# Kernel optimization log

Measured on AMD Instinct MI355X. Metric: run time of the kernel, lower is better.

## Reference

```python
import jax, jax.numpy as jnp
import numpy as np

H, W, SCALE = 480, 640, 8  # full-res grid and coarse downsample factor (hw0_i/hw0_c)


def _struct_feats(pts, anchor_ids):
    """pts: [N, H*W, 3]; anchor_ids: [N, A] int -> [N, L, 4*A] with L=(H//SCALE)*(W//SCALE)."""
    N = pts.shape[0]
    coarse = pts.reshape(N, H, W, 3)[:, ::SCALE, ::SCALE, :].reshape(N, -1, 3)  # [N, L, 3]
    anchors = jnp.take_along_axis(pts, anchor_ids[:, :, None], axis=1)          # [N, A, 3]
    diff = coarse[:, :, None, :] - anchors[:, None, :, :]                        # [N, L, A, 3]
    dist = jnp.sum(diff * diff, axis=-1, keepdims=True)                          # [N, L, A, 1]
    s = jnp.concatenate([diff, dist], axis=-1)                                   # [N, L, A, 4]
    s = s / jnp.sum(jnp.abs(s), axis=-2, keepdims=True)                          # L1 norm over anchor axis
    s = jnp.swapaxes(s, -1, -2).reshape(N, coarse.shape[1], -1)                  # [N, L, 4A]
    return s


def _mlp(x, W1, b1, W2, b2):
    return jax.nn.relu(x @ W1 + b1) @ W2 + b2


def setup_inputs() -> dict:
    key = jax.random.key(0)
    ks = jax.random.split(key, 10)
    N, L, C, A, P = 4, 4800, 256, 128, H * W
    D = C + 4 * A  # 768
    return {
        "feat0": jax.random.normal(ks[0], (N, L, C), jnp.float32),
        "feat1": jax.random.normal(ks[1], (N, L, C), jnp.float32),
        "pts_3d0": jax.random.normal(ks[2], (N, P, 3), jnp.float32),
        "pts_3d1": jax.random.normal(ks[3], (N, P, 3), jnp.float32),
        "anchor_i_ids": jax.random.randint(ks[4], (N, A), 0, P),
        "anchor_j_ids": jax.random.randint(ks[5], (N, A), 0, P),
        "W1": jax.random.normal(ks[6], (D, D), jnp.float32) * (1.0 / np.sqrt(D)),
        "b1": jnp.zeros((D,), jnp.float32),
        "W2": jax.random.normal(ks[7], (D, C), jnp.float32) * (1.0 / np.sqrt(D)),
        "b2": jnp.zeros((C,), jnp.float32),
    }


def reference(feat0, feat1, pts_3d0, pts_3d1, anchor_i_ids, anchor_j_ids, W1, b1, W2, b2):
    s0 = _struct_feats(pts_3d0, anchor_i_ids)  # [N, L, 4A]
    s1 = _struct_feats(pts_3d1, anchor_j_ids)
    aug0 = _mlp(jnp.concatenate([feat0, s0], axis=-1), W1, b1, W2, b2)  # [N, L, C]
    aug1 = _mlp(jnp.concatenate([feat1, s1], axis=-1), W1, b1, W2, b2)
    return (aug0, aug1)
```

## Files before the change

kernel.cpp:

```cpp
#include <hip/hip_runtime.h>
#include <stdint.h>
#include <stddef.h>

typedef __attribute__((ext_vector_type(8))) short short8;
typedef __attribute__((ext_vector_type(4))) short short4v;
typedef __attribute__((ext_vector_type(4))) float f32x4;

typedef const __attribute__((address_space(3))) char* lds_cp;

#define GLDS16(gp, lp)                                                        \
    __builtin_amdgcn_global_load_lds(                                         \
        (const __attribute__((address_space(1))) void*)(gp),                  \
        (__attribute__((address_space(3))) void*)(lp), 16, 0, 0)

__device__ __forceinline__ short8 ldsr16(lds_cp p) {
    short8 v;
    asm volatile("ds_read_b128 %0, %1" : "=v"(v) : "v"(p));
    return v;
}

template <int N>
__device__ __forceinline__ void wait_lgkm() {
    static_assert(N == 0 || N == 2 || N == 4 || N == 8, "unsupported count");
    if constexpr (N == 0) asm volatile("s_waitcnt lgkmcnt(0)" ::: "memory");
    else if constexpr (N == 2) asm volatile("s_waitcnt lgkmcnt(2)" ::: "memory");
    else if constexpr (N == 4) asm volatile("s_waitcnt lgkmcnt(4)" ::: "memory");
    else if constexpr (N == 8) asm volatile("s_waitcnt lgkmcnt(8)" ::: "memory");
    __builtin_amdgcn_sched_barrier(0);
}

__device__ __forceinline__ unsigned short f2bf(float f) {
    union { float f; uint32_t u; } v;
    v.f = f;
    uint32_t u = v.u;
    u += 0x7FFFu + ((u >> 16) & 1u);
    return (unsigned short)(u >> 16);
}

__global__ __launch_bounds__(1024) void transpose_to_bf16(
    const float* __restrict__ src, unsigned short* __restrict__ dst, int R, int C)
{
    __shared__ float tile[32][33];
    const int c0 = blockIdx.x * 32, r0 = blockIdx.y * 32;
    const int tx = threadIdx.x, ty = threadIdx.y;
    tile[ty][tx] = src[(size_t)(r0 + ty) * C + (c0 + tx)];
    __syncthreads();
    dst[(size_t)(c0 + ty) * R + (r0 + tx)] = f2bf(tile[tx][ty]);
}

__global__ __launch_bounds__(64) void struct_pack(
    const float* __restrict__ feat0, const float* __restrict__ feat1,
    const float* __restrict__ pts0,  const float* __restrict__ pts1,
    const int* __restrict__ ids0,    const int* __restrict__ ids1,
    unsigned short* __restrict__ xw)
{
    const int m = blockIdx.x;
    const int t = m / 19200;
    const int r = m % 19200;
    const int n = r / 4800;
    const int l = r % 4800;
    const float* feat = t ? feat1 : feat0;
    const float* pts  = (t ? pts1 : pts0) + (size_t)n * (307200 * 3);
    const int*   ids  = (t ? ids1 : ids0) + n * 128;
    const int a = threadIdx.x;

    const int lr = l / 80, lc = l % 80;
    const int p  = (lr * 8) * 640 + lc * 8;
    const float cx = pts[p * 3 + 0], cy = pts[p * 3 + 1], cz = pts[p * 3 + 2];

    const int id0 = ids[a], id1 = ids[a + 64];
    const float d0x = cx - pts[id0 * 3 + 0];
    const float d0y = cy - pts[id0 * 3 + 1];
    const float d0z = cz - pts[id0 * 3 + 2];
    const float d0d = d0x * d0x + d0y * d0y + d0z * d0z;
    const float d1x = cx - pts[id1 * 3 + 0];
    const float d1y = cy - pts[id1 * 3 + 1];
    const float d1z = cz - pts[id1 * 3 + 2];
    const float d1d = d1x * d1x + d1y * d1y + d1z * d1z;

    float p0 = fabsf(d0x) + fabsf(d1x);
    float p1 = fabsf(d0y) + fabsf(d1y);
    float p2 = fabsf(d0z) + fabsf(d1z);
    float p3 = d0d + d1d;
#pragma unroll
    for (int off = 32; off; off >>= 1) {
        p0 += __shfl_xor(p0, off);
        p1 += __shfl_xor(p1, off);
        p2 += __shfl_xor(p2, off);
        p3 += __shfl_xor(p3, off);
    }
    const float i0 = 1.0f / p0, i1 = 1.0f / p1, i2 = 1.0f / p2, i3 = 1.0f / p3;

    unsigned short* xrow = xw + (size_t)m * 768;
    const float* frow = feat + (size_t)(n * 4800 + l) * 256;
    const float4 fv = ((const float4*)frow)[a];
    short4v s4;
    s4.x = (short)f2bf(fv.x); s4.y = (short)f2bf(fv.y);
    s4.z = (short)f2bf(fv.z); s4.w = (short)f2bf(fv.w);
    *(short4v*)(xrow + a * 4) = s4;

    xrow[256 + 0 * 128 + a]      = f2bf(d0x * i0);
    xrow[256 + 0 * 128 + a + 64] = f2bf(d1x * i0);
    xrow[256 + 1 * 128 + a]      = f2bf(d0y * i1);
    xrow[256 + 1 * 128 + a + 64] = f2bf(d1y * i1);
    xrow[256 + 2 * 128 + a]      = f2bf(d0z * i2);
    xrow[256 + 2 * 128 + a + 64] = f2bf(d1z * i2);
    xrow[256 + 3 * 128 + a]      = f2bf(d0d * i3);
    xrow[256 + 3 * 128 + a + 64] = f2bf(d1d * i3);
}

template <int MI, int NJ, int WRN_LOG, bool RELU, bool OUT_BF16>
__global__ __launch_bounds__(512, 2) void gemm_t(
    const unsigned short* __restrict__ A,
    const unsigned short* __restrict__ Bt,
    const float* __restrict__ bias,
    void* __restrict__ Cout,
    int K, int N, int ntx, int q8, int r8)
{
    constexpr int WRN = 1 << WRN_LOG;
    constexpr int WRM = 8 / WRN;
    constexpr int BM = WRM * MI * 16;
    constexpr int BN = WRN * NJ * 16;
    constexpr int ASLOT = BM * 128;
    constexpr int BSLOT = BN * 128;
    constexpr int ALD = BM / 64;
    constexpr int BLD = BN / 64;
    static_assert(ALD == 4, "vmcnt immediates assume 4 A-loads/wave/tile");
    static_assert(MI + NJ <= 13, "lgkm in-flight cap");

    extern __shared__ char lds[];
    const int nt = K >> 6;

    const int bid = blockIdx.x;
    const int xcd = bid & 7, idx = bid >> 3;
    const int w = (xcd < r8 ? xcd * (q8 + 1) : r8 * (q8 + 1) + (xcd - r8) * q8) + idx;
    const int n0 = (w % ntx) * BN;
    const int m0 = (w / ntx) * BM;

    const int tid = threadIdx.x;
    const int lane = tid & 63;
    const int wv = tid >> 6;
    const int wr = wv >> WRN_LOG;
    const int wc = wv & (WRN - 1);

    const int slr = lane >> 3;
    const int kc  = (lane & 7) ^ slr;
    const unsigned short* gA = A  + (size_t)(m0 + wv * 8 + slr) * K + kc * 8;
    const unsigned short* gB = Bt + (size_t)(n0 + wv * 8 + slr) * K + kc * 8;

    auto stA = [&](int slot, int i, int kt) {
        GLDS16(gA + (size_t)i * 64 * K + kt, lds + slot * ASLOT + (i * 64 + wv * 8) * 128);
    };
    auto stB = [&](int slot, int j, int kt) {
        GLDS16(gB + (size_t)j * 64 * K + kt, lds + 3 * ASLOT + slot * BSLOT + (j * 64 + wv * 8) * 128);
    };

    const int rsel = lane & 15;
    const int kbh  = lane >> 4;
    const int ck0 = ((kbh) ^ (rsel & 7)) * 16;
    const int ck1 = ((4 + kbh) ^ (rsel & 7)) * 16;
    const int aRowB = (wr * (MI * 16) + rsel) * 128;
    const int bRowB = (wc * (NJ * 16) + rsel) * 128;

    auto LDA = [&](int slot, int mi, int ks) -> short8 {
        return ldsr16((lds_cp)(lds + slot * ASLOT + aRowB + mi * 2048 + (ks ? ck1 : ck0)));
    };
    auto LDB = [&](int slot, int nj, int ks) -> short8 {
        return ldsr16((lds_cp)(lds + 3 * ASLOT + slot * BSLOT + bRowB + nj * 2048 + (ks ? ck1 : ck0)));
    };

    f32x4 acc[MI][NJ] = {};
    short8 aL[MI / 2], aH[MI / 2], aL1[MI / 2], aH1[MI / 2], bF0[NJ], bF1[NJ];

    {
#pragma unroll
        for (int i = 0; i < ALD; ++i) stA(0, i, 0);
#pragma unroll
        for (int j = 0; j < BLD; ++j) stB(0, j, 0);
        if (nt > 1) {
#pragma unroll
            for (int i = 0; i < ALD; ++i) stA(1, i, 64);
            asm volatile("s_waitcnt vmcnt(4)" ::: "memory");
        } else {
            asm volatile("s_waitcnt vmcnt(0)" ::: "memory");
        }
        __builtin_amdgcn_s_barrier();
    }

    int cb3 = 0;
    for (int t = 0; t < nt; ++t) {
        const int cb2 = t & 1;
        const int sb2 = cb2 ^ 1;
        int sa3 = cb3 + 2; if (sa3 >= 3) sa3 -= 3;
        const int kt1 = (t + 1) << 6;
        const int kt2 = (t + 2) << 6;
        const bool stb = (t + 1) < nt;
        const bool sta = (t + 2) < nt;

#pragma unroll
        for (int nj = 0; nj < NJ; ++nj) bF0[nj] = LDB(cb2, nj, 0);
#pragma unroll
        for (int mi = 0; mi < MI / 2; ++mi) aL[mi] = LDA(cb3, mi, 0);
#pragma unroll
        for (int mi = 0; mi < MI / 2; ++mi) aH[mi] = LDA(cb3, MI / 2 + mi, 0);

        wait_lgkm<MI / 2>();
        __builtin_amdgcn_s_setprio(1);
#pragma unroll
        for (int mi = 0; mi < MI / 2; ++mi)
#pragma unroll
            for (int nj = 0; nj < NJ; ++nj)
                acc[mi][nj] = __builtin_amdgcn_mfma_f32_16x16x32_bf16(aL[mi], bF0[nj], acc[mi][nj], 0, 0, 0);
        __builtin_amdgcn_s_setprio(0);

#pragma unroll
        for (int nj = 0; nj < NJ; ++nj) bF1[nj] = LDB(cb2, nj, 1);
        if (stb) {
#pragma unroll
            for (int j = 0; j < BLD; ++j) stB(sb2, j, kt1);
        }

        wait_lgkm<NJ>();
        __builtin_amdgcn_s_setprio(1);
#pragma unroll
        for (int mi = 0; mi < MI / 2; ++mi)
#pragma unroll
            for (int nj = 0; nj < NJ; ++nj)
                acc[MI / 2 + mi][nj] = __builtin_amdgcn_mfma_f32_16x16x32_bf16(aH[mi], bF0[nj], acc[MI / 2 + mi][nj], 0, 0, 0);
        __builtin_amdgcn_s_setprio(0);

#pragma unroll
        for (int mi = 0; mi < MI / 2; ++mi) aL1[mi] = LDA(cb3, mi, 1);
#pragma unroll
        for (int mi = 0; mi < MI / 2; ++mi) aH1[mi] = LDA(cb3, MI / 2 + mi, 1);
        if (sta) {
            stA(sa3, 0, kt2); stA(sa3, 1, kt2); stA(sa3, 2, kt2); stA(sa3, 3, kt2);
        }

        wait_lgkm<MI / 2>();
        __builtin_amdgcn_s_setprio(1);
#pragma unroll
        for (int mi = 0; mi < MI / 2; ++mi)
#pragma unroll
            for (int nj = 0; nj < NJ; ++nj)
                acc[mi][nj] = __builtin_amdgcn_mfma_f32_16x16x32_bf16(aL1[mi], bF1[nj], acc[mi][nj], 0, 0, 0);
        __builtin_amdgcn_s_setprio(0);

        wait_lgkm<0>();
        __builtin_amdgcn_s_setprio(1);
#pragma unroll
        for (int mi = 0; mi < MI / 2; ++mi)
#pragma unroll
            for (int nj = 0; nj < NJ; ++nj)
                acc[MI / 2 + mi][nj] = __builtin_amdgcn_mfma_f32_16x16x32_bf16(aH1[mi], bF1[nj], acc[MI / 2 + mi][nj], 0, 0, 0);
        __builtin_amdgcn_s_setprio(0);

        if (t + 1 < nt) {
            if (sta) asm volatile("s_waitcnt vmcnt(4)" ::: "memory");
            else     asm volatile("s_waitcnt vmcnt(0)" ::: "memory");
            __builtin_amdgcn_s_barrier();
        }
        cb3 = (cb3 + 1 == 3) ? 0 : cb3 + 1;
    }

    const int crow = (lane >> 4) * 4;
    const int ccol = lane & 15;
#pragma unroll
    for (int nj = 0; nj < NJ; ++nj) {
        const int col = n0 + wc * (NJ * 16) + nj * 16 + ccol;
        const float bv = bias[col];
#pragma unroll
        for (int mi = 0; mi < MI; ++mi) {
#pragma unroll
            for (int rg = 0; rg < 4; ++rg) {
                const int row = m0 + wr * (MI * 16) + mi * 16 + crow + rg;
                float v = acc[mi][nj][rg] + bv;
                if (RELU) v = fmaxf(v, 0.0f);
                if (OUT_BF16) {
                    ((unsigned short*)Cout)[(size_t)row * N + col] = f2bf(v);
                } else {
                    ((float*)Cout)[(size_t)row * N + col] = v;
                }
            }
        }
    }
}

extern "C" void kernel_launch(void* const* d_in, const int* in_sizes, int n_in,
                              void* d_out, int out_size, void* d_ws, size_t ws_size,
                              hipStream_t stream) {
    const float* feat0 = (const float*)d_in[0];
    const float* feat1 = (const float*)d_in[1];
    const float* pts0  = (const float*)d_in[2];
    const float* pts1  = (const float*)d_in[3];
    const int*   ids0  = (const int*)d_in[4];
    const int*   ids1  = (const int*)d_in[5];
    const float* W1    = (const float*)d_in[6];
    const float* b1    = (const float*)d_in[7];
    const float* W2    = (const float*)d_in[8];
    const float* b2    = (const float*)d_in[9];
    float* out = (float*)d_out;

    char* ws = (char*)d_ws;
    unsigned short* xw  = (unsigned short*)(ws);
    unsigned short* h   = (unsigned short*)(ws + 58982400);
    unsigned short* w1t = (unsigned short*)(ws + 117964800);
    unsigned short* w2t = (unsigned short*)(ws + 119144448);

    const int LDS1 = 3 * 32768 + 2 * 32768;
    const int LDS2 = 3 * 32768 + 2 * 16384;
    (void)hipFuncSetAttribute((const void*)&gemm_t<8, 4, 2, true, true>,
                              hipFuncAttributeMaxDynamicSharedMemorySize, LDS1);
    (void)hipFuncSetAttribute((const void*)&gemm_t<4, 4, 1, false, false>,
                              hipFuncAttributeMaxDynamicSharedMemorySize, LDS2);

    dim3 tb(32, 32);
    transpose_to_bf16<<<dim3(768 / 32, 768 / 32), tb, 0, stream>>>(W1, w1t, 768, 768);
    transpose_to_bf16<<<dim3(256 / 32, 768 / 32), tb, 0, stream>>>(W2, w2t, 768, 256);

    struct_pack<<<38400, 64, 0, stream>>>(feat0, feat1, pts0, pts1, ids0, ids1, xw);

    gemm_t<8, 4, 2, true, true><<<450, 512, LDS1, stream>>>(xw, w1t, b1, (void*)h, 768, 768, 3, 56, 2);
    gemm_t<4, 4, 1, false, false><<<300, 512, LDS2, stream>>>(h, w2t, b2, (void*)out, 768, 256, 2, 37, 4);
}
```

Measured before the change: 116.9 us.

## Unify GEMMs on a 256x128 tile with 4 waves and K-step of 32

Both MLP GEMMs now use a single 256x128 block tile run by 4 waves (each wave computes 128x64), with the K step halved from 64 to 32. The LDS layout and swizzle are rebuilt for 64-byte rows, and the per-iteration schedule is simplified to one batch of fragment loads followed by two MFMA phases. The first GEMM goes from 450 large blocks to 900 smaller ones, and the LDS footprint shrinks, which should allow more resident blocks. In exchange each block does more barriers per unit of work and has less data reuse per wave than the larger 8-wave tile.

```diff
diff --git a/kernel.cpp b/kernel.cpp
--- a/kernel.cpp
+++ b/kernel.cpp
@@ -21,11 +21,9 @@
 
 template <int N>
 __device__ __forceinline__ void wait_lgkm() {
-    static_assert(N == 0 || N == 2 || N == 4 || N == 8, "unsupported count");
+    static_assert(N == 0 || N == 4, "unsupported count");
     if constexpr (N == 0) asm volatile("s_waitcnt lgkmcnt(0)" ::: "memory");
-    else if constexpr (N == 2) asm volatile("s_waitcnt lgkmcnt(2)" ::: "memory");
-    else if constexpr (N == 4) asm volatile("s_waitcnt lgkmcnt(4)" ::: "memory");
-    else if constexpr (N == 8) asm volatile("s_waitcnt lgkmcnt(8)" ::: "memory");
+    else asm volatile("s_waitcnt lgkmcnt(4)" ::: "memory");
     __builtin_amdgcn_sched_barrier(0);
 }
 
@@ -109,77 +107,65 @@
     xrow[256 + 3 * 128 + a + 64] = f2bf(d1d * i3);
 }
 
-template <int MI, int NJ, int WRN_LOG, bool RELU, bool OUT_BF16>
-__global__ __launch_bounds__(512, 2) void gemm_t(
+template <bool RELU, bool OUT_BF16>
+__global__ __launch_bounds__(256, 2) void gemm_t(
     const unsigned short* __restrict__ A,
     const unsigned short* __restrict__ Bt,
     const float* __restrict__ bias,
     void* __restrict__ Cout,
     int K, int N, int ntx, int q8, int r8)
 {
-    constexpr int WRN = 1 << WRN_LOG;
-    constexpr int WRM = 8 / WRN;
-    constexpr int BM = WRM * MI * 16;
-    constexpr int BN = WRN * NJ * 16;
-    constexpr int ASLOT = BM * 128;
-    constexpr int BSLOT = BN * 128;
-    constexpr int ALD = BM / 64;
-    constexpr int BLD = BN / 64;
-    static_assert(ALD == 4, "vmcnt immediates assume 4 A-loads/wave/tile");
-    static_assert(MI + NJ <= 13, "lgkm in-flight cap");
-
+    constexpr int ASLOT = 256 * 64;
+    constexpr int BSLOT = 128 * 64;
     extern __shared__ char lds[];
-    const int nt = K >> 6;
+    char* ldsB = lds + 3 * ASLOT;
+    const int nt = K >> 5;
 
     const int bid = blockIdx.x;
     const int xcd = bid & 7, idx = bid >> 3;
     const int w = (xcd < r8 ? xcd * (q8 + 1) : r8 * (q8 + 1) + (xcd - r8) * q8) + idx;
-    const int n0 = (w % ntx) * BN;
-    const int m0 = (w / ntx) * BM;
+    const int n0 = (w % ntx) * 128;
+    const int m0 = (w / ntx) * 256;
 
     const int tid = threadIdx.x;
     const int lane = tid & 63;
     const int wv = tid >> 6;
-    const int wr = wv >> WRN_LOG;
-    const int wc = wv & (WRN - 1);
-
-    const int slr = lane >> 3;
-    const int kc  = (lane & 7) ^ slr;
-    const unsigned short* gA = A  + (size_t)(m0 + wv * 8 + slr) * K + kc * 8;
-    const unsigned short* gB = Bt + (size_t)(n0 + wv * 8 + slr) * K + kc * 8;
+    const int wr = wv >> 1;
+    const int wc = wv & 1;
+
+    const int lrow = lane >> 2;
+    const int lchk = (lane & 3) ^ ((lane >> 3) & 3);
+    const unsigned short* gA = A  + (size_t)(m0 + wv * 64 + lrow) * K + lchk * 8;
+    const unsigned short* gB = Bt + (size_t)(n0 + wv * 32 + lrow) * K + lchk * 8;
 
     auto stA = [&](int slot, int i, int kt) {
-        GLDS16(gA + (size_t)i * 64 * K + kt, lds + slot * ASLOT + (i * 64 + wv * 8) * 128);
+        GLDS16(gA + (size_t)i * 16 * K + kt, lds + slot * ASLOT + (wv * 4 + i) * 1024);
     };
     auto stB = [&](int slot, int j, int kt) {
-        GLDS16(gB + (size_t)j * 64 * K + kt, lds + 3 * ASLOT + slot * BSLOT + (j * 64 + wv * 8) * 128);
-    };
-
-    const int rsel = lane & 15;
-    const int kbh  = lane >> 4;
-    const int ck0 = ((kbh) ^ (rsel & 7)) * 16;
-    const int ck1 = ((4 + kbh) ^ (rsel & 7)) * 16;
-    const int aRowB = (wr * (MI * 16) + rsel) * 128;
-    const int bRowB = (wc * (NJ * 16) + rsel) * 128;
-
-    auto LDA = [&](int slot, int mi, int ks) -> short8 {
-        return ldsr16((lds_cp)(lds + slot * ASLOT + aRowB + mi * 2048 + (ks ? ck1 : ck0)));
-    };
-    auto LDB = [&](int slot, int nj, int ks) -> short8 {
-        return ldsr16((lds_cp)(lds + 3 * ASLOT + slot * BSLOT + bRowB + nj * 2048 + (ks ? ck1 : ck0)));
-    };
-
-    f32x4 acc[MI][NJ] = {};
-    short8 aL[MI / 2], aH[MI / 2], aL1[MI / 2], aH1[MI / 2], bF0[NJ], bF1[NJ];
+        GLDS16(gB + (size_t)j * 16 * K + kt, ldsB + slot * BSLOT + (wv * 2 + j) * 1024);
+    };
+
+    const int R = lane & 15;
+    const int q = lane >> 4;
+    const int ck = (q ^ ((R >> 1) & 3)) * 16;
+    const int aOff = (wr * 128 + R) * 64 + ck;
+    const int bOff = (wc * 64 + R) * 64 + ck;
+
+    auto LDA = [&](int slot, int mi) -> short8 {
+        return ldsr16((lds_cp)(lds + slot * ASLOT + aOff + mi * 1024));
+    };
+    auto LDB = [&](int slot, int nj) -> short8 {
+        return ldsr16((lds_cp)(ldsB + slot * BSLOT + bOff + nj * 1024));
+    };
+
+    f32x4 acc[8][4] = {};
+    short8 aF[8], bF[4];
 
     {
-#pragma unroll
-        for (int i = 0; i < ALD; ++i) stA(0, i, 0);
-#pragma unroll
-        for (int j = 0; j < BLD; ++j) stB(0, j, 0);
+        stA(0, 0, 0); stA(0, 1, 0); stA(0, 2, 0); stA(0, 3, 0);
+        stB(0, 0, 0); stB(0, 1, 0);
         if (nt > 1) {
-#pragma unroll
-            for (int i = 0; i < ALD; ++i) stA(1, i, 64);
+            stA(1, 0, 32); stA(1, 1, 32); stA(1, 2, 32); stA(1, 3, 32);
             asm volatile("s_waitcnt vmcnt(4)" ::: "memory");
         } else {
             asm volatile("s_waitcnt vmcnt(0)" ::: "memory");
@@ -192,67 +178,34 @@
         const int cb2 = t & 1;
         const int sb2 = cb2 ^ 1;
         int sa3 = cb3 + 2; if (sa3 >= 3) sa3 -= 3;
-        const int kt1 = (t + 1) << 6;
-        const int kt2 = (t + 2) << 6;
+        const int kt1 = (t + 1) << 5;
+        const int kt2 = (t + 2) << 5;
         const bool stb = (t + 1) < nt;
         const bool sta = (t + 2) < nt;
 
-#pragma unroll
-        for (int nj = 0; nj < NJ; ++nj) bF0[nj] = LDB(cb2, nj, 0);
-#pragma unroll
-        for (int mi = 0; mi < MI / 2; ++mi) aL[mi] = LDA(cb3, mi, 0);
-#pragma unroll
-        for (int mi = 0; mi < MI / 2; ++mi) aH[mi] = LDA(cb3, MI / 2 + mi, 0);
-
-        wait_lgkm<MI / 2>();
+        bF[0] = LDB(cb2, 0); bF[1] = LDB(cb2, 1); bF[2] = LDB(cb2, 2); bF[3] = LDB(cb2, 3);
+        aF[0] = LDA(cb3, 0); aF[1] = LDA(cb3, 1); aF[2] = LDA(cb3, 2); aF[3] = LDA(cb3, 3);
+        if (stb) { stB(sb2, 0, kt1); stB(sb2, 1, kt1); }
+
+        aF[4] = LDA(cb3, 4); aF[5] = LDA(cb3, 5); aF[6] = LDA(cb3, 6); aF[7] = LDA(cb3, 7);
+        if (sta) { stA(sa3, 0, kt2); stA(sa3, 1, kt2); stA(sa3, 2, kt2); stA(sa3, 3, kt2); }
+
+        wait_lgkm<4>();
         __builtin_amdgcn_s_setprio(1);
 #pragma unroll
-        for (int mi = 0; mi < MI / 2; ++mi)
-#pragma unroll
-            for (int nj = 0; nj < NJ; ++nj)
-                acc[mi][nj] = __builtin_amdgcn_mfma_f32_16x16x32_bf16(aL[mi], bF0[nj], acc[mi][nj], 0, 0, 0);
-        __builtin_amdgcn_s_setprio(0);
-
-#pragma unroll
-        for (int nj = 0; nj < NJ; ++nj) bF1[nj] = LDB(cb2, nj, 1);
-        if (stb) {
-#pragma unroll
-            for (int j = 0; j < BLD; ++j) stB(sb2, j, kt1);
-        }
-
-        wait_lgkm<NJ>();
-        __builtin_amdgcn_s_setprio(1);
-#pragma unroll
-        for (int mi = 0; mi < MI / 2; ++mi)
-#pragma unroll
-            for (int nj = 0; nj < NJ; ++nj)
-                acc[MI / 2 + mi][nj] = __builtin_amdgcn_mfma_f32_16x16x32_bf16(aH[mi], bF0[nj], acc[MI / 2 + mi][nj], 0, 0, 0);
-        __builtin_amdgcn_s_setprio(0);
-
-#pragma unroll
-        for (int mi = 0; mi < MI / 2; ++mi) aL1[mi] = LDA(cb3, mi, 1);
-#pragma unroll
-        for (int mi = 0; mi < MI / 2; ++mi) aH1[mi] = LDA(cb3, MI / 2 + mi, 1);
-        if (sta) {
-            stA(sa3, 0, kt2); stA(sa3, 1, kt2); stA(sa3, 2, kt2); stA(sa3, 3, kt2);
-        }
-
-        wait_lgkm<MI / 2>();
-        __builtin_amdgcn_s_setprio(1);
-#pragma unroll
-        for (int mi = 0; mi < MI / 2; ++mi)
-#pragma unroll
-            for (int nj = 0; nj < NJ; ++nj)
-                acc[mi][nj] = __builtin_amdgcn_mfma_f32_16x16x32_bf16(aL1[mi], bF1[nj], acc[mi][nj], 0, 0, 0);
+        for (int mi = 0; mi < 4; ++mi)
+#pragma unroll
+            for (int nj = 0; nj < 4; ++nj)
+                acc[mi][nj] = __builtin_amdgcn_mfma_f32_16x16x32_bf16(aF[mi], bF[nj], acc[mi][nj], 0, 0, 0);
         __builtin_amdgcn_s_setprio(0);
 
         wait_lgkm<0>();
         __builtin_amdgcn_s_setprio(1);
 #pragma unroll
-        for (int mi = 0; mi < MI / 2; ++mi)
-#pragma unroll
-            for (int nj = 0; nj < NJ; ++nj)
-                acc[MI / 2 + mi][nj] = __builtin_amdgcn_mfma_f32_16x16x32_bf16(aH1[mi], bF1[nj], acc[MI / 2 + mi][nj], 0, 0, 0);
+        for (int mi = 4; mi < 8; ++mi)
+#pragma unroll
+            for (int nj = 0; nj < 4; ++nj)
+                acc[mi][nj] = __builtin_amdgcn_mfma_f32_16x16x32_bf16(aF[mi], bF[nj], acc[mi][nj], 0, 0, 0);
         __builtin_amdgcn_s_setprio(0);
 
         if (t + 1 < nt) {
@@ -266,14 +219,14 @@
     const int crow = (lane >> 4) * 4;
     const int ccol = lane & 15;
 #pragma unroll
-    for (int nj = 0; nj < NJ; ++nj) {
-        const int col = n0 + wc * (NJ * 16) + nj * 16 + ccol;
+    for (int nj = 0; nj < 4; ++nj) {
+        const int col = n0 + wc * 64 + nj * 16 + ccol;
         const float bv = bias[col];
 #pragma unroll
-        for (int mi = 0; mi < MI; ++mi) {
+        for (int mi = 0; mi < 8; ++mi) {
 #pragma unroll
             for (int rg = 0; rg < 4; ++rg) {
-                const int row = m0 + wr * (MI * 16) + mi * 16 + crow + rg;
+                const int row = m0 + wr * 128 + mi * 16 + crow + rg;
                 float v = acc[mi][nj][rg] + bv;
                 if (RELU) v = fmaxf(v, 0.0f);
                 if (OUT_BF16) {
@@ -307,12 +260,11 @@
     unsigned short* w1t = (unsigned short*)(ws + 117964800);
     unsigned short* w2t = (unsigned short*)(ws + 119144448);
 
-    const int LDS1 = 3 * 32768 + 2 * 32768;
-    const int LDS2 = 3 * 32768 + 2 * 16384;
-    (void)hipFuncSetAttribute((const void*)&gemm_t<8, 4, 2, true, true>,
-                              hipFuncAttributeMaxDynamicSharedMemorySize, LDS1);
-    (void)hipFuncSetAttribute((const void*)&gemm_t<4, 4, 1, false, false>,
-                              hipFuncAttributeMaxDynamicSharedMemorySize, LDS2);
+    const int LDS = 3 * 16384 + 2 * 8192;
+    (void)hipFuncSetAttribute((const void*)&gemm_t<true, true>,
+                              hipFuncAttributeMaxDynamicSharedMemorySize, LDS);
+    (void)hipFuncSetAttribute((const void*)&gemm_t<false, false>,
+                              hipFuncAttributeMaxDynamicSharedMemorySize, LDS);
 
     dim3 tb(32, 32);
     transpose_to_bf16<<<dim3(768 / 32, 768 / 32), tb, 0, stream>>>(W1, w1t, 768, 768);
@@ -320,6 +272,6 @@
 
     struct_pack<<<38400, 64, 0, stream>>>(feat0, feat1, pts0, pts1, ids0, ids1, xw);
 
-    gemm_t<8, 4, 2, true, true><<<450, 512, LDS1, stream>>>(xw, w1t, b1, (void*)h, 768, 768, 3, 56, 2);
-    gemm_t<4, 4, 1, false, false><<<300, 512, LDS2, stream>>>(h, w2t, b2, (void*)out, 768, 256, 2, 37, 4);
-}
+    gemm_t<true, true><<<900, 256, LDS, stream>>>(xw, w1t, b1, (void*)h, 768, 768, 6, 112, 4);
+    gemm_t<false, false><<<300, 256, LDS, stream>>>(h, w2t, b2, (void*)out, 768, 256, 2, 37, 4);
+}
```

Result: no change. 116.0 us (-0.8%).

## Switch GEMM inner loop to 32x32x16 bf16 MFMA with 2x4 wave grid

Applied to the files above, without the earlier changes.

Replaces the 16x16x32 MFMA tiles with 32x32x16 MFMA tiles and a fixed 2x4 wave layout (each wave covers 128 rows by BFR*32 columns). The K-step of 64 is now split into four 16-wide substeps with double-buffered fragment registers and adjusted LDS swizzle offsets and wait counts. The aim is fewer LDS fragment reads per FLOP and higher MFMA throughput per instruction. The cost is larger accumulator register footprint and a different epilogue row mapping.

```diff
diff --git a/kernel.cpp b/kernel.cpp
--- a/kernel.cpp
+++ b/kernel.cpp
@@ -4,7 +4,7 @@
 
 typedef __attribute__((ext_vector_type(8))) short short8;
 typedef __attribute__((ext_vector_type(4))) short short4v;
-typedef __attribute__((ext_vector_type(4))) float f32x4;
+typedef __attribute__((ext_vector_type(16))) float f32x16;
 
 typedef const __attribute__((address_space(3))) char* lds_cp;
 
@@ -21,11 +21,10 @@
 
 template <int N>
 __device__ __forceinline__ void wait_lgkm() {
-    static_assert(N == 0 || N == 2 || N == 4 || N == 8, "unsupported count");
+    static_assert(N == 0 || N == 5 || N == 6, "unsupported count");
     if constexpr (N == 0) asm volatile("s_waitcnt lgkmcnt(0)" ::: "memory");
-    else if constexpr (N == 2) asm volatile("s_waitcnt lgkmcnt(2)" ::: "memory");
-    else if constexpr (N == 4) asm volatile("s_waitcnt lgkmcnt(4)" ::: "memory");
-    else if constexpr (N == 8) asm volatile("s_waitcnt lgkmcnt(8)" ::: "memory");
+    else if constexpr (N == 5) asm volatile("s_waitcnt lgkmcnt(5)" ::: "memory");
+    else if constexpr (N == 6) asm volatile("s_waitcnt lgkmcnt(6)" ::: "memory");
     __builtin_amdgcn_sched_barrier(0);
 }
 
@@ -109,7 +108,7 @@
     xrow[256 + 3 * 128 + a + 64] = f2bf(d1d * i3);
 }
 
-template <int MI, int NJ, int WRN_LOG, bool RELU, bool OUT_BF16>
+template <int AFR, int BFR, bool RELU, bool OUT_BF16>
 __global__ __launch_bounds__(512, 2) void gemm_t(
     const unsigned short* __restrict__ A,
     const unsigned short* __restrict__ Bt,
@@ -117,18 +116,17 @@
     void* __restrict__ Cout,
     int K, int N, int ntx, int q8, int r8)
 {
-    constexpr int WRN = 1 << WRN_LOG;
-    constexpr int WRM = 8 / WRN;
-    constexpr int BM = WRM * MI * 16;
-    constexpr int BN = WRN * NJ * 16;
+    constexpr int BM = 2 * AFR * 32;
+    constexpr int BN = 4 * BFR * 32;
     constexpr int ASLOT = BM * 128;
     constexpr int BSLOT = BN * 128;
     constexpr int ALD = BM / 64;
     constexpr int BLD = BN / 64;
+    constexpr int PERKS = AFR + BFR;
     static_assert(ALD == 4, "vmcnt immediates assume 4 A-loads/wave/tile");
-    static_assert(MI + NJ <= 13, "lgkm in-flight cap");
 
     extern __shared__ char lds[];
+    char* ldsB = lds + 3 * ASLOT;
     const int nt = K >> 6;
 
     const int bid = blockIdx.x;
@@ -140,8 +138,8 @@
     const int tid = threadIdx.x;
     const int lane = tid & 63;
     const int wv = tid >> 6;
-    const int wr = wv >> WRN_LOG;
-    const int wc = wv & (WRN - 1);
+    const int wr = wv >> 2;
+    const int wc = wv & 3;
 
     const int slr = lane >> 3;
     const int kc  = (lane & 7) ^ slr;
@@ -152,25 +150,26 @@
         GLDS16(gA + (size_t)i * 64 * K + kt, lds + slot * ASLOT + (i * 64 + wv * 8) * 128);
     };
     auto stB = [&](int slot, int j, int kt) {
-        GLDS16(gB + (size_t)j * 64 * K + kt, lds + 3 * ASLOT + slot * BSLOT + (j * 64 + wv * 8) * 128);
+        GLDS16(gB + (size_t)j * 64 * K + kt, ldsB + slot * BSLOT + (j * 64 + wv * 8) * 128);
     };
 
-    const int rsel = lane & 15;
-    const int kbh  = lane >> 4;
-    const int ck0 = ((kbh) ^ (rsel & 7)) * 16;
-    const int ck1 = ((4 + kbh) ^ (rsel & 7)) * 16;
-    const int aRowB = (wr * (MI * 16) + rsel) * 128;
-    const int bRowB = (wc * (NJ * 16) + rsel) * 128;
+    const int R32 = lane & 31;
+    const int hi  = lane >> 5;
+    int ck[4];
+#pragma unroll
+    for (int ks = 0; ks < 4; ++ks) ck[ks] = (((ks * 2 + hi) ^ (R32 & 7)) * 16);
+    const int aBase = (wr * 128 + R32) * 128;
+    const int bBase = (wc * (BFR * 32) + R32) * 128;
 
     auto LDA = [&](int slot, int mi, int ks) -> short8 {
-        return ldsr16((lds_cp)(lds + slot * ASLOT + aRowB + mi * 2048 + (ks ? ck1 : ck0)));
+        return ldsr16((lds_cp)(lds + slot * ASLOT + aBase + mi * 4096 + ck[ks]));
     };
     auto LDB = [&](int slot, int nj, int ks) -> short8 {
-        return ldsr16((lds_cp)(lds + 3 * ASLOT + slot * BSLOT + bRowB + nj * 2048 + (ks ? ck1 : ck0)));
+        return ldsr16((lds_cp)(ldsB + slot * BSLOT + bBase + nj * 4096 + ck[ks]));
     };
 
-    f32x4 acc[MI][NJ] = {};
-    short8 aL[MI / 2], aH[MI / 2], aL1[MI / 2], aH1[MI / 2], bF0[NJ], bF1[NJ];
+    f32x16 acc[AFR][BFR] = {};
+    short8 aF[2][AFR], bF[2][BFR];
 
     {
 #pragma unroll
@@ -198,61 +197,63 @@
         const bool sta = (t + 2) < nt;
 
 #pragma unroll
-        for (int nj = 0; nj < NJ; ++nj) bF0[nj] = LDB(cb2, nj, 0);
-#pragma unroll
-        for (int mi = 0; mi < MI / 2; ++mi) aL[mi] = LDA(cb3, mi, 0);
-#pragma unroll
-        for (int mi = 0; mi < MI / 2; ++mi) aH[mi] = LDA(cb3, MI / 2 + mi, 0);
-
-        wait_lgkm<MI / 2>();
-        __builtin_amdgcn_s_setprio(1);
-#pragma unroll
-        for (int mi = 0; mi < MI / 2; ++mi)
-#pragma unroll
-            for (int nj = 0; nj < NJ; ++nj)
-                acc[mi][nj] = __builtin_amdgcn_mfma_f32_16x16x32_bf16(aL[mi], bF0[nj], acc[mi][nj], 0, 0, 0);
-        __builtin_amdgcn_s_setprio(0);
-
-#pragma unroll
-        for (int nj = 0; nj < NJ; ++nj) bF1[nj] = LDB(cb2, nj, 1);
+        for (int mi = 0; mi < AFR; ++mi) aF[0][mi] = LDA(cb3, mi, 0);
+#pragma unroll
+        for (int nj = 0; nj < BFR; ++nj) bF[0][nj] = LDB(cb2, nj, 0);
+#pragma unroll
+        for (int mi = 0; mi < AFR; ++mi) aF[1][mi] = LDA(cb3, mi, 1);
+#pragma unroll
+        for (int nj = 0; nj < BFR; ++nj) bF[1][nj] = LDB(cb2, nj, 1);
         if (stb) {
 #pragma unroll
             for (int j = 0; j < BLD; ++j) stB(sb2, j, kt1);
         }
 
-        wait_lgkm<NJ>();
+        wait_lgkm<PERKS>();
         __builtin_amdgcn_s_setprio(1);
 #pragma unroll
-        for (int mi = 0; mi < MI / 2; ++mi)
-#pragma unroll
-            for (int nj = 0; nj < NJ; ++nj)
-                acc[MI / 2 + mi][nj] = __builtin_amdgcn_mfma_f32_16x16x32_bf16(aH[mi], bF0[nj], acc[MI / 2 + mi][nj], 0, 0, 0);
+        for (int mi = 0; mi < AFR; ++mi)
+#pragma unroll
+            for (int nj = 0; nj < BFR; ++nj)
+                acc[mi][nj] = __builtin_amdgcn_mfma_f32_32x32x16_bf16(aF[0][mi], bF[0][nj], acc[mi][nj], 0, 0, 0);
         __builtin_amdgcn_s_setprio(0);
 
 #pragma unroll
-        for (int mi = 0; mi < MI / 2; ++mi) aL1[mi] = LDA(cb3, mi, 1);
-#pragma unroll
-        for (int mi = 0; mi < MI / 2; ++mi) aH1[mi] = LDA(cb3, MI / 2 + mi, 1);
-        if (sta) {
-            stA(sa3, 0, kt2); stA(sa3, 1, kt2); stA(sa3, 2, kt2); stA(sa3, 3, kt2);
-        }
-
-        wait_lgkm<MI / 2>();
+        for (int mi = 0; mi < AFR; ++mi) aF[0][mi] = LDA(cb3, mi, 2);
+#pragma unroll
+        for (int nj = 0; nj < BFR; ++nj) bF[0][nj] = LDB(cb2, nj, 2);
+        if (sta) { stA(sa3, 0, kt2); stA(sa3, 1, kt2); stA(sa3, 2, kt2); stA(sa3, 3, kt2); }
+
+        wait_lgkm<PERKS>();
         __builtin_amdgcn_s_setprio(1);
 #pragma unroll
-        for (int mi = 0; mi < MI / 2; ++mi)
-#pragma unroll
-            for (int nj = 0; nj < NJ; ++nj)
-                acc[mi][nj] = __builtin_amdgcn_mfma_f32_16x16x32_bf16(aL1[mi], bF1[nj], acc[mi][nj], 0, 0, 0);
+        for (int mi = 0; mi < AFR; ++mi)
+#pragma unroll
+            for (int nj = 0; nj < BFR; ++nj)
+                acc[mi][nj] = __builtin_amdgcn_mfma_f32_32x32x16_bf16(aF[1][mi], bF[1][nj], acc[mi][nj], 0, 0, 0);
+        __builtin_amdgcn_s_setprio(0);
+
+#pragma unroll
+        for (int mi = 0; mi < AFR; ++mi) aF[1][mi] = LDA(cb3, mi, 3);
+#pragma unroll
+        for (int nj = 0; nj < BFR; ++nj) bF[1][nj] = LDB(cb2, nj, 3);
+
+        wait_lgkm<PERKS>();
+        __builtin_amdgcn_s_setprio(1);
+#pragma unroll
+        for (int mi = 0; mi < AFR; ++mi)
+#pragma unroll
+            for (int nj = 0; nj < BFR; ++nj)
+                acc[mi][nj] = __builtin_amdgcn_mfma_f32_32x32x16_bf16(aF[0][mi], bF[0][nj], acc[mi][nj], 0, 0, 0);
         __builtin_amdgcn_s_setprio(0);
 
         wait_lgkm<0>();
         __builtin_amdgcn_s_setprio(1);
 #pragma unroll
-        for (int mi = 0; mi < MI / 2; ++mi)
-#pragma unroll
-            for (int nj = 0; nj < NJ; ++nj)
-                acc[MI / 2 + mi][nj] = __builtin_amdgcn_mfma_f32_16x16x32_bf16(aH1[mi], bF1[nj], acc[MI / 2 + mi][nj], 0, 0, 0);
+        for (int mi = 0; mi < AFR; ++mi)
+#pragma unroll
+            for (int nj = 0; nj < BFR; ++nj)
+                acc[mi][nj] = __builtin_amdgcn_mfma_f32_32x32x16_bf16(aF[1][mi], bF[1][nj], acc[mi][nj], 0, 0, 0);
         __builtin_amdgcn_s_setprio(0);
 
         if (t + 1 < nt) {
@@ -263,17 +264,16 @@
         cb3 = (cb3 + 1 == 3) ? 0 : cb3 + 1;
     }
 
-    const int crow = (lane >> 4) * 4;
-    const int ccol = lane & 15;
-#pragma unroll
-    for (int nj = 0; nj < NJ; ++nj) {
-        const int col = n0 + wc * (NJ * 16) + nj * 16 + ccol;
+    const int ccol = lane & 31;
+#pragma unroll
+    for (int nj = 0; nj < BFR; ++nj) {
+        const int col = n0 + wc * (BFR * 32) + nj * 32 + ccol;
         const float bv = bias[col];
 #pragma unroll
-        for (int mi = 0; mi < MI; ++mi) {
-#pragma unroll
-            for (int rg = 0; rg < 4; ++rg) {
-                const int row = m0 + wr * (MI * 16) + mi * 16 + crow + rg;
+        for (int mi = 0; mi < AFR; ++mi) {
+#pragma unroll
+            for (int rg = 0; rg < 16; ++rg) {
+                const int row = m0 + wr * 128 + mi * 32 + (rg & 3) + 8 * (rg >> 2) + 4 * hi;
                 float v = acc[mi][nj][rg] + bv;
                 if (RELU) v = fmaxf(v, 0.0f);
                 if (OUT_BF16) {
@@ -309,9 +309,9 @@
 
     const int LDS1 = 3 * 32768 + 2 * 32768;
     const int LDS2 = 3 * 32768 + 2 * 16384;
-    (void)hipFuncSetAttribute((const void*)&gemm_t<8, 4, 2, true, true>,
+    (void)hipFuncSetAttribute((const void*)&gemm_t<4, 2, true, true>,
                               hipFuncAttributeMaxDynamicSharedMemorySize, LDS1);
-    (void)hipFuncSetAttribute((const void*)&gemm_t<4, 4, 1, false, false>,
+    (void)hipFuncSetAttribute((const void*)&gemm_t<4, 1, false, false>,
                               hipFuncAttributeMaxDynamicSharedMemorySize, LDS2);
 
     dim3 tb(32, 32);
@@ -320,6 +320,6 @@
 
     struct_pack<<<38400, 64, 0, stream>>>(feat0, feat1, pts0, pts1, ids0, ids1, xw);
 
-    gemm_t<8, 4, 2, true, true><<<450, 512, LDS1, stream>>>(xw, w1t, b1, (void*)h, 768, 768, 3, 56, 2);
-    gemm_t<4, 4, 1, false, false><<<300, 512, LDS2, stream>>>(h, w2t, b2, (void*)out, 768, 256, 2, 37, 4);
-}
+    gemm_t<4, 2, true, true><<<450, 512, LDS1, stream>>>(xw, w1t, b1, (void*)h, 768, 768, 3, 56, 2);
+    gemm_t<4, 1, false, false><<<300, 512, LDS2, stream>>>(h, w2t, b2, (void*)out, 768, 256, 2, 37, 4);
+}
```

Result: slower. 120.6 us (+3.2%).
